# Kernel tuning notes

Hardware: AMD Instinct MI355X
Metric: run time of the kernel (lower is better)

## Reference

```python
import jax, jax.numpy as jnp
import numpy as np

B, N, FEAT, HID, CTX = 16384, 7, 512, 256, 256
COMB = N * HID + CTX  # 2048


def setup_inputs() -> dict:
    key = jax.random.key(0)
    ks = jax.random.split(key, 20)
    s = lambda k, shape, sc=0.05: jax.random.normal(k, shape, dtype=jnp.float32) * sc
    adj = jax.random.randint(ks[1], (N, N), 0, 2).astype(jnp.float32)
    # guarantee self-loops so no row is fully masked (still exercise nan_to_num path robustly)
    adj = jnp.maximum(adj, jnp.eye(N, dtype=jnp.float32))
    return {
        "node_feats": jax.random.normal(ks[0], (B, N, FEAT), dtype=jnp.float32),
        "adj": adj,
        "context": jax.random.normal(ks[2], (B, CTX), dtype=jnp.float32),
        "base_preds": jax.random.normal(ks[3], (B, 5), dtype=jnp.float32),
        "W1": s(ks[4], (HID, FEAT)),
        "a1": s(ks[5], (1, 2 * HID)),
        "W2": s(ks[6], (HID, HID)),
        "a2": s(ks[7], (1, 2 * HID)),
        "wh1_w": s(ks[8], (32, COMB)), "wh1_b": s(ks[9], (32,)),
        "wh2_w": s(ks[10], (16, 32)), "wh2_b": s(ks[11], (16,)),
        "wh3_w": s(ks[12], (5, 16)), "wh3_b": s(ks[13], (5,)),
        "rh1_w": s(ks[14], (16, COMB)), "rh1_b": s(ks[15], (16,)),
        "rh2_w": s(ks[16], (1, 16)), "rh2_b": s(ks[17], (1,)),
    }


def _gat_layer(x, adj, W, a):
    # x: (B, N, in_dim); W: (D, in_dim); a: (1, 2D)
    h = jnp.einsum('bni,di->bnd', x, W)  # (B, N, D)
    D = W.shape[0]
    # a([h_i, h_j]) == h_i @ a[:, :D] + h_j @ a[:, D:]
    s_i = h @ a[0, :D]   # (B, N)
    s_j = h @ a[0, D:]   # (B, N)
    e = s_i[:, :, None] + s_j[:, None, :]          # (B, N, N)
    e = jax.nn.leaky_relu(e, negative_slope=0.2)
    e = jnp.where(adj[None] == 0, -jnp.inf, e)
    alpha = jax.nn.softmax(e, axis=-1)
    alpha = jnp.nan_to_num(alpha, nan=0.0)
    out = jnp.einsum('bij,bjd->bid', alpha, h)     # (B, N, D)
    return out, alpha


def reference(node_feats, adj, context, base_preds, W1, a1, W2, a2,
              wh1_w, wh1_b, wh2_w, wh2_b, wh3_w, wh3_b,
              rh1_w, rh1_b, rh2_w, rh2_b):
    h, _attn1 = _gat_layer(node_feats, adj, W1, a1)
    h = jax.nn.relu(h)
    h, attn2 = _gat_layer(h, adj, W2, a2)
    h = jax.nn.relu(h)
    graph_embed = h.reshape(h.shape[0], -1)                 # (B, N*D)
    combined = jnp.concatenate([graph_embed, context], -1)  # (B, COMB)
    # weight head (dropout is inference-mode identity)
    t = jax.nn.relu(combined @ wh1_w.T + wh1_b)
    t = jax.nn.relu(t @ wh2_w.T + wh2_b)
    raw_weights = t @ wh3_w.T + wh3_b                       # (B, 5)
    weights = jax.nn.softmax(raw_weights, axis=-1)
    weighted_pred = jnp.sum(weights * base_preds, axis=-1)  # (B,)
    r = jnp.tanh(combined @ rh1_w.T + rh1_b)
    residual = (r @ rh2_w.T + rh2_b)[:, 0] * 0.05
    pred = jnp.maximum(weighted_pred + residual, 0.05)
    return pred, weights, attn2
```

## Files before the change

### kernel.cpp

```cpp
#include <hip/hip_runtime.h>

#define B_SZ 16384
#define NN 7
#define HID 256
#define COMB 2048

typedef __attribute__((ext_vector_type(8))) short short8;
typedef __attribute__((ext_vector_type(4))) float floatx4;
typedef __attribute__((ext_vector_type(4))) unsigned short ushortx4;
typedef unsigned short us;

__device__ __forceinline__ float bf2f(us u) {
    union { unsigned int i; float f; } v; v.i = ((unsigned int)u) << 16; return v.f;
}
__device__ __forceinline__ us f2bf(float f) {
    union { unsigned int i; float f; } v; v.f = f;
    return (us)((v.i + 0x7FFFu + ((v.i >> 16) & 1u)) >> 16);
}
__device__ __forceinline__ us f2bf_fast(float f) {
    union { unsigned int i; float f; } v; v.f = f;
    return (us)((v.i + 0x8000u) >> 16);
}
__device__ __forceinline__ void gl_lds16(const us* g, us* l) {
    __builtin_amdgcn_global_load_lds(
        (const __attribute__((address_space(1))) unsigned int*)g,
        (__attribute__((address_space(3))) unsigned int*)l, 16, 0, 0);
}

__global__ __launch_bounds__(256) void pack_weights(const float* __restrict__ W1,
                                                    const float* __restrict__ W2,
                                                    const float* __restrict__ wh1,
                                                    const float* __restrict__ rh1,
                                                    us* __restrict__ dst) {
    int i = (blockIdx.x * 256 + threadIdx.x) * 4;
    if (i >= 294912) return;
    const float* src; int off;
    if (i < 131072)      { src = W1;  off = i; }
    else if (i < 196608) { src = W2;  off = i - 131072; }
    else if (i < 262144) { src = wh1; off = i - 196608; }
    else                 { src = rh1; off = i - 262144; }
    floatx4 v = *(const floatx4*)(src + off);
    ushortx4 o = {f2bf(v[0]), f2bf(v[1]), f2bf(v[2]), f2bf(v[3])};
    *(ushortx4*)(dst + i) = o;
}

template <int SRC_STRIDE, bool WRITE_ALPHA>
__device__ __forceinline__ void attn_graph(const us* hb, const float* adjs, const float* avec,
                                           us* dst, int dstStride, float* alpha_dst, int lane) {
    float hv[NN][4];
#pragma unroll
    for (int n = 0; n < NN; ++n) {
        ushortx4 r = *(const ushortx4*)(hb + n * SRC_STRIDE + lane * 4);
        hv[n][0] = bf2f(r[0]); hv[n][1] = bf2f(r[1]);
        hv[n][2] = bf2f(r[2]); hv[n][3] = bf2f(r[3]);
    }
    floatx4 ai = *(const floatx4*)(avec + lane * 4);
    floatx4 aj = *(const floatx4*)(avec + HID + lane * 4);
    float si[NN], sj[NN];
#pragma unroll
    for (int n = 0; n < NN; ++n) {
        float pi = hv[n][0] * ai[0] + hv[n][1] * ai[1] + hv[n][2] * ai[2] + hv[n][3] * ai[3];
        float pj = hv[n][0] * aj[0] + hv[n][1] * aj[1] + hv[n][2] * aj[2] + hv[n][3] * aj[3];
#pragma unroll
        for (int off = 32; off; off >>= 1) {
            pi += __shfl_xor(pi, off);
            pj += __shfl_xor(pj, off);
        }
        si[n] = pi; sj[n] = pj;
    }
    const int j = lane & 7;
    float sjm = sj[0];
    if (j == 1) sjm = sj[1];
    if (j == 2) sjm = sj[2];
    if (j == 3) sjm = sj[3];
    if (j == 4) sjm = sj[4];
    if (j == 5) sjm = sj[5];
    if (j == 6) sjm = sj[6];
    const int jc = (j < 7) ? j : 0;
    float alpha[NN];
#pragma unroll
    for (int i = 0; i < NN; ++i) {
        float x = si[i] + sjm;
        x = (x >= 0.f) ? x : 0.2f * x;
        bool ok = (j < 7) && (adjs[i * 7 + jc] != 0.f);
        float e = ok ? x : -1e30f;
        float m = e;
        m = fmaxf(m, __shfl_xor(m, 1, 8));
        m = fmaxf(m, __shfl_xor(m, 2, 8));
        m = fmaxf(m, __shfl_xor(m, 4, 8));
        float ex = ok ? __expf(e - m) : 0.f;
        float s = ex;
        s += __shfl_xor(s, 1, 8);
        s += __shfl_xor(s, 2, 8);
        s += __shfl_xor(s, 4, 8);
        alpha[i] = (s > 0.f) ? ex * __frcp_rn(s) : 0.f;
    }
    if (WRITE_ALPHA && lane < 7) {
#pragma unroll
        for (int i = 0; i < NN; ++i) alpha_dst[i * NN + lane] = alpha[i];
    }
#pragma unroll
    for (int i = 0; i < NN; ++i) {
        floatx4 o = (floatx4){0.f, 0.f, 0.f, 0.f};
#pragma unroll
        for (int jj = 0; jj < NN; ++jj) {
            float a = __shfl(alpha[i], jj, 8);
            o[0] += a * hv[jj][0]; o[1] += a * hv[jj][1];
            o[2] += a * hv[jj][2]; o[3] += a * hv[jj][3];
        }
        ushortx4 st = {f2bf(fmaxf(o[0], 0.f)), f2bf(fmaxf(o[1], 0.f)),
                       f2bf(fmaxf(o[2], 0.f)), f2bf(fmaxf(o[3], 0.f))};
        *(ushortx4*)(dst + i * dstStride + lane * 4) = st;
    }
}

__global__ __launch_bounds__(512) void fused_g1(const float* __restrict__ Af,
                                                const us* __restrict__ W1b,
                                                const float* __restrict__ adj,
                                                const float* __restrict__ avec,
                                                us* __restrict__ x2g) {
    extern __shared__ __attribute__((aligned(16))) char smem[];
    us* As = (us*)smem;
    us* Bs = (us*)(smem + 7168);
    us* hs = (us*)(smem + 23552);
    float* adjs = (float*)(smem + 80896);

    const int tid = threadIdx.x;
    const int wave = tid >> 6, lane = tid & 63;
    const int quad = lane >> 4, m16 = lane & 15;
    const long rowBase = (long)blockIdx.x * 112;
    if (tid < 49) adjs[tid] = adj[tid];

    floatx4 acc[7][2];
#pragma unroll
    for (int rt = 0; rt < 7; ++rt)
#pragma unroll
        for (int ct = 0; ct < 2; ++ct) acc[rt][ct] = (floatx4){0.f, 0.f, 0.f, 0.f};

    for (int k0 = 0; k0 < 512; k0 += 32) {
        if (tid < 448) {
            int r = tid >> 2, kh = tid & 3;
            const floatx4* src = (const floatx4*)(Af + (rowBase + r) * 512 + k0 + kh * 8);
            floatx4 v0 = src[0], v1 = src[1];
            short8 s;
            s[0] = f2bf_fast(v0[0]); s[1] = f2bf_fast(v0[1]);
            s[2] = f2bf_fast(v0[2]); s[3] = f2bf_fast(v0[3]);
            s[4] = f2bf_fast(v1[0]); s[5] = f2bf_fast(v1[1]);
            s[6] = f2bf_fast(v1[2]); s[7] = f2bf_fast(v1[3]);
            *(short8*)&As[(r >> 4) * 512 + (kh * 16 + (r & 15)) * 8] = s;
        }
        {
            int b1 = wave * 16, b2 = 128 + wave * 16;
            gl_lds16(W1b + (long)(b1 + (lane & 15)) * 512 + k0 + (lane >> 4) * 8, &Bs[b1 * 32]);
            gl_lds16(W1b + (long)(b2 + (lane & 15)) * 512 + k0 + (lane >> 4) * 8, &Bs[b2 * 32]);
        }
        __syncthreads();
        short8 af[7], bf[2];
#pragma unroll
        for (int rt = 0; rt < 7; ++rt)
            af[rt] = *(const short8*)&As[rt * 512 + (quad * 16 + m16) * 8];
#pragma unroll
        for (int ct = 0; ct < 2; ++ct)
            bf[ct] = *(const short8*)&Bs[(wave * 2 + ct) * 512 + (quad * 16 + m16) * 8];
#pragma unroll
        for (int rt = 0; rt < 7; ++rt)
#pragma unroll
            for (int ct = 0; ct < 2; ++ct)
                acc[rt][ct] = __builtin_amdgcn_mfma_f32_16x16x32_bf16(af[rt], bf[ct], acc[rt][ct], 0, 0, 0);
        __syncthreads();
    }
#pragma unroll
    for (int rt = 0; rt < 7; ++rt)
#pragma unroll
        for (int ct = 0; ct < 2; ++ct)
#pragma unroll
            for (int i = 0; i < 4; ++i)
                hs[(rt * 16 + quad * 4 + i) * 256 + wave * 32 + ct * 16 + m16] = f2bf(acc[rt][ct][i]);
    __syncthreads();
#pragma unroll
    for (int gg = 0; gg < 2; ++gg) {
        int gl = wave * 2 + gg;
        long b = (long)blockIdx.x * 16 + gl;
        attn_graph<256, false>(&hs[gl * 7 * 256], adjs, avec,
                               x2g + b * 7 * 256, 256, nullptr, lane);
    }
}

__global__ __launch_bounds__(512) void fused_rest(const us* __restrict__ x2g,
                                                  const us* __restrict__ W2b,
                                                  const us* __restrict__ Whb,
                                                  const float* __restrict__ adj,
                                                  const float* __restrict__ avec,
                                                  const float* __restrict__ context,
                                                  const float* __restrict__ wh1_b,
                                                  const float* __restrict__ wh2_w,
                                                  const float* __restrict__ wh2_b,
                                                  const float* __restrict__ wh3_w,
                                                  const float* __restrict__ wh3_b,
                                                  const float* __restrict__ rh1_b,
                                                  const float* __restrict__ rh2_w,
                                                  const float* __restrict__ rh2_b,
                                                  const float* __restrict__ base_preds,
                                                  float* __restrict__ out) {
    extern __shared__ __attribute__((aligned(16))) char smem[];
    us* As = (us*)smem;
    us* Bs = (us*)(smem + 8192);
    us* hs = (us*)(smem + 24576);
    us* ctxs = (us*)(smem + 82816);
    float* red = (float*)(smem + 91136);
    float* fin = (float*)(smem + 115712);
    float* adjs = (float*)(smem + 118784);

    const int tid = threadIdx.x;
    const int wave = tid >> 6, lane = tid & 63;
    const int quad = lane >> 4, m16 = lane & 15;
    const long rowBase = (long)blockIdx.x * 112;
    const long gbase = (long)blockIdx.x * 16;
    if (tid < 49) adjs[tid] = adj[tid];
    {
        int r = tid >> 5, c = (tid & 31) * 8;
        const floatx4* src = (const floatx4*)(context + (gbase + r) * 256 + c);
        floatx4 v0 = src[0], v1 = src[1];
        short8 s;
        s[0] = f2bf(v0[0]); s[1] = f2bf(v0[1]); s[2] = f2bf(v0[2]); s[3] = f2bf(v0[3]);
        s[4] = f2bf(v1[0]); s[5] = f2bf(v1[1]); s[6] = f2bf(v1[2]); s[7] = f2bf(v1[3]);
        *(short8*)&ctxs[r * 260 + c] = s;
    }

    floatx4 acc[7][2];
#pragma unroll
    for (int rt = 0; rt < 7; ++rt)
#pragma unroll
        for (int ct = 0; ct < 2; ++ct) acc[rt][ct] = (floatx4){0.f, 0.f, 0.f, 0.f};

    for (int k0 = 0; k0 < 256; k0 += 32) {
        gl_lds16(x2g + (rowBase + wave * 16 + (lane & 15)) * 256 + k0 + (lane >> 4) * 8,
                 &As[wave * 512]);
        {
            int b1 = wave * 16, b2 = 128 + wave * 16;
            gl_lds16(W2b + (long)(b1 + (lane & 15)) * 256 + k0 + (lane >> 4) * 8, &Bs[b1 * 32]);
            gl_lds16(W2b + (long)(b2 + (lane & 15)) * 256 + k0 + (lane >> 4) * 8, &Bs[b2 * 32]);
        }
        __syncthreads();
        short8 af[7], bf[2];
#pragma unroll
        for (int rt = 0; rt < 7; ++rt)
            af[rt] = *(const short8*)&As[rt * 512 + (quad * 16 + m16) * 8];
#pragma unroll
        for (int ct = 0; ct < 2; ++ct)
            bf[ct] = *(const short8*)&Bs[(wave * 2 + ct) * 512 + (quad * 16 + m16) * 8];
#pragma unroll
        for (int rt = 0; rt < 7; ++rt)
#pragma unroll
            for (int ct = 0; ct < 2; ++ct)
                acc[rt][ct] = __builtin_amdgcn_mfma_f32_16x16x32_bf16(af[rt], bf[ct], acc[rt][ct], 0, 0, 0);
        __syncthreads();
    }
#pragma unroll
    for (int rt = 0; rt < 7; ++rt)
#pragma unroll
        for (int ct = 0; ct < 2; ++ct)
#pragma unroll
            for (int i = 0; i < 4; ++i)
                hs[(rt * 16 + quad * 4 + i) * 260 + wave * 32 + ct * 16 + m16] = f2bf(acc[rt][ct][i]);
    __syncthreads();
    float* alf = out + 6 * B_SZ;
#pragma unroll
    for (int gg = 0; gg < 2; ++gg) {
        int gl = wave * 2 + gg;
        long b = gbase + gl;
        attn_graph<260, true>(&hs[gl * 7 * 260], adjs, avec,
                              &hs[gl * 7 * 260], 260, alf + b * 49, lane);
    }
    __syncthreads();
    floatx4 acc3[3];
#pragma unroll
    for (int ct = 0; ct < 3; ++ct) acc3[ct] = (floatx4){0.f, 0.f, 0.f, 0.f};
    const long wk = (long)wave * 256;
#pragma unroll
    for (int s = 0; s < 8; ++s) {
        int kk = s * 32;
        short8 a;
        if (wave < 7) a = *(const short8*)&hs[(m16 * 7 + wave) * 260 + kk + quad * 8];
        else          a = *(const short8*)&ctxs[m16 * 260 + kk + quad * 8];
#pragma unroll
        for (int ct = 0; ct < 3; ++ct) {
            short8 bh = *(const short8*)(Whb + (long)(ct * 16 + m16) * COMB + wk + kk + quad * 8);
            acc3[ct] = __builtin_amdgcn_mfma_f32_16x16x32_bf16(a, bh, acc3[ct], 0, 0, 0);
        }
    }
#pragma unroll
    for (int ct = 0; ct < 3; ++ct)
#pragma unroll
        for (int i = 0; i < 4; ++i)
            red[wave * 768 + (quad * 4 + i) * 48 + ct * 16 + m16] = acc3[ct][i];
    __syncthreads();
    {
        float s = 0.f;
#pragma unroll
        for (int w = 0; w < 8; ++w) s += red[w * 768 + tid];
        fin[tid] = s;
        if (tid < 256) {
            float s2 = 0.f;
#pragma unroll
            for (int w = 0; w < 8; ++w) s2 += red[w * 768 + 512 + tid];
            fin[512 + tid] = s2;
        }
    }
    __syncthreads();
    if (tid < 16) {
        const int g = tid;
        const long b = gbase + g;
        const float* g48 = &fin[g * 48];
        float t1[32], r1[16];
#pragma unroll
        for (int k = 0; k < 32; ++k) t1[k] = fmaxf(g48[k] + wh1_b[k], 0.f);
#pragma unroll
        for (int k = 0; k < 16; ++k) r1[k] = tanhf(g48[32 + k] + rh1_b[k]);
        float t2[16];
#pragma unroll
        for (int jj = 0; jj < 16; ++jj) {
            float s = wh2_b[jj];
            for (int k = 0; k < 32; ++k) s += wh2_w[jj * 32 + k] * t1[k];
            t2[jj] = fmaxf(s, 0.f);
        }
        float rw[5], m = -1e30f;
#pragma unroll
        for (int o = 0; o < 5; ++o) {
            float s = wh3_b[o];
            for (int jj = 0; jj < 16; ++jj) s += wh3_w[o * 16 + jj] * t2[jj];
            rw[o] = s; m = fmaxf(m, s);
        }
        float se = 0.f;
#pragma unroll
        for (int o = 0; o < 5; ++o) { rw[o] = __expf(rw[o] - m); se += rw[o]; }
        float inv = 1.f / se, wp = 0.f;
#pragma unroll
        for (int o = 0; o < 5; ++o) {
            float w = rw[o] * inv;
            out[B_SZ + b * 5 + o] = w;
            wp += w * base_preds[b * 5 + o];
        }
        float rs = rh2_b[0];
#pragma unroll
        for (int k = 0; k < 16; ++k) rs += rh2_w[k] * r1[k];
        out[b] = fmaxf(wp + rs * 0.05f, 0.05f);
    }
}

extern "C" void kernel_launch(void* const* d_in, const int* in_sizes, int n_in,
                              void* d_out, int out_size, void* d_ws, size_t ws_size,
                              hipStream_t stream) {
    const float* node_feats = (const float*)d_in[0];
    const float* adj        = (const float*)d_in[1];
    const float* context    = (const float*)d_in[2];
    const float* base_preds = (const float*)d_in[3];
    const float* W1         = (const float*)d_in[4];
    const float* a1         = (const float*)d_in[5];
    const float* W2         = (const float*)d_in[6];
    const float* a2         = (const float*)d_in[7];
    const float* wh1_w = (const float*)d_in[8];
    const float* wh1_b = (const float*)d_in[9];
    const float* wh2_w = (const float*)d_in[10];
    const float* wh2_b = (const float*)d_in[11];
    const float* wh3_w = (const float*)d_in[12];
    const float* wh3_b = (const float*)d_in[13];
    const float* rh1_w = (const float*)d_in[14];
    const float* rh1_b = (const float*)d_in[15];
    const float* rh2_w = (const float*)d_in[16];
    const float* rh2_b = (const float*)d_in[17];
    float* out = (float*)d_out;

    char* ws = (char*)d_ws;
    const size_t HB = (size_t)B_SZ * NN * HID * 2;
    us* x2  = (us*)ws;
    us* W1b = (us*)(ws + HB);
    us* W2b = W1b + 131072;
    us* Whb = W2b + 65536;

    pack_weights<<<288, 256, 0, stream>>>(W1, W2, wh1_w, rh1_w, W1b);

    fused_g1<<<1024, 512, 81104, stream>>>(node_feats, W1b, adj, a1, x2);

    fused_rest<<<1024, 512, 118992, stream>>>(x2, W2b, Whb, adj, a2, context,
                                              wh1_b, wh2_w, wh2_b, wh3_w, wh3_b,
                                              rh1_b, rh2_w, rh2_b, base_preds, out);
}
```

Before: 541.7 us.

## Halve per-block tile to 8 graphs, read weights from global, raise occupancy

Both fused kernels now process 8 graphs (56 rows) per block instead of 16, over twice as many blocks. LDS use drops sharply: weight tiles are no longer staged in shared memory and each wave reads its B fragments straight from global/L2. The K step grows to 64 and launch bounds request 4 blocks per CU. The aim is more resident waves to hide memory latency, at the cost of more redundant global weight reads and a 64-row MFMA tile where only 56 rows are useful.

```diff
diff --git a/kernel.cpp b/kernel.cpp
--- a/kernel.cpp
+++ b/kernel.cpp
@@ -114,204 +114,185 @@
     }
 }
 
-__global__ __launch_bounds__(512) void fused_g1(const float* __restrict__ Af,
-                                                const us* __restrict__ W1b,
-                                                const float* __restrict__ adj,
-                                                const float* __restrict__ avec,
-                                                us* __restrict__ x2g) {
-    extern __shared__ __attribute__((aligned(16))) char smem[];
-    us* As = (us*)smem;
-    us* Bs = (us*)(smem + 7168);
-    us* hs = (us*)(smem + 23552);
-    float* adjs = (float*)(smem + 80896);
-
+
+__global__ __launch_bounds__(512, 4) void fused_g1(const float* __restrict__ Af,
+                                                   const us* __restrict__ W1b,
+                                                   const float* __restrict__ adj,
+                                                   const float* __restrict__ avec,
+                                                   us* __restrict__ x2g) {
+    __shared__ __attribute__((aligned(16))) us As[4096];
+    __shared__ __attribute__((aligned(16))) us hs[56 * 264];
+    __shared__ float adjs[52];
     const int tid = threadIdx.x;
     const int wave = tid >> 6, lane = tid & 63;
     const int quad = lane >> 4, m16 = lane & 15;
-    const long rowBase = (long)blockIdx.x * 112;
+    const long rowBase = (long)blockIdx.x * 56;
     if (tid < 49) adjs[tid] = adj[tid];
 
-    floatx4 acc[7][2];
-#pragma unroll
-    for (int rt = 0; rt < 7; ++rt)
+    floatx4 acc[4][2];
+#pragma unroll
+    for (int rt = 0; rt < 4; ++rt)
 #pragma unroll
         for (int ct = 0; ct < 2; ++ct) acc[rt][ct] = (floatx4){0.f, 0.f, 0.f, 0.f};
 
-    for (int k0 = 0; k0 < 512; k0 += 32) {
-        if (tid < 448) {
-            int r = tid >> 2, kh = tid & 3;
-            const floatx4* src = (const floatx4*)(Af + (rowBase + r) * 512 + k0 + kh * 8);
-            floatx4 v0 = src[0], v1 = src[1];
-            short8 s;
-            s[0] = f2bf_fast(v0[0]); s[1] = f2bf_fast(v0[1]);
-            s[2] = f2bf_fast(v0[2]); s[3] = f2bf_fast(v0[3]);
-            s[4] = f2bf_fast(v1[0]); s[5] = f2bf_fast(v1[1]);
-            s[6] = f2bf_fast(v1[2]); s[7] = f2bf_fast(v1[3]);
-            *(short8*)&As[(r >> 4) * 512 + (kh * 16 + (r & 15)) * 8] = s;
-        }
-        {
-            int b1 = wave * 16, b2 = 128 + wave * 16;
-            gl_lds16(W1b + (long)(b1 + (lane & 15)) * 512 + k0 + (lane >> 4) * 8, &Bs[b1 * 32]);
-            gl_lds16(W1b + (long)(b2 + (lane & 15)) * 512 + k0 + (lane >> 4) * 8, &Bs[b2 * 32]);
-        }
+    const int r = tid >> 3, kq8 = tid & 7;
+    long rowA = rowBase + r; if (rowA > 114687) rowA = 114687;
+    const float* aptr = Af + rowA * 512 + kq8 * 8;
+    us* wdst = &As[((r >> 3) * 64 + (r & 7) * 8 + kq8) * 8];
+    const int colb = wave * 32;
+
+    for (int s = 0; s < 8; ++s) {
+        const int k0 = s * 64;
+        floatx4 v0 = *(const floatx4*)(aptr + k0);
+        floatx4 v1 = *(const floatx4*)(aptr + k0 + 4);
+        short8 sv;
+        sv[0] = f2bf_fast(v0[0]); sv[1] = f2bf_fast(v0[1]);
+        sv[2] = f2bf_fast(v0[2]); sv[3] = f2bf_fast(v0[3]);
+        sv[4] = f2bf_fast(v1[0]); sv[5] = f2bf_fast(v1[1]);
+        sv[6] = f2bf_fast(v1[2]); sv[7] = f2bf_fast(v1[3]);
+        *(short8*)wdst = sv;
         __syncthreads();
-        short8 af[7], bf[2];
-#pragma unroll
-        for (int rt = 0; rt < 7; ++rt)
-            af[rt] = *(const short8*)&As[rt * 512 + (quad * 16 + m16) * 8];
+#pragma unroll
+        for (int t = 0; t < 2; ++t) {
+            short8 b0 = *(const short8*)(W1b + (long)(colb + m16) * 512 + k0 + t * 32 + quad * 8);
+            short8 b1 = *(const short8*)(W1b + (long)(colb + 16 + m16) * 512 + k0 + t * 32 + quad * 8);
+            short8 a[4];
+#pragma unroll
+            for (int rt = 0; rt < 4; ++rt)
+                a[rt] = *(const short8*)&As[((rt * 2 + (m16 >> 3)) * 64 + (m16 & 7) * 8 + t * 4 + quad) * 8];
+#pragma unroll
+            for (int rt = 0; rt < 4; ++rt) {
+                acc[rt][0] = __builtin_amdgcn_mfma_f32_16x16x32_bf16(a[rt], b0, acc[rt][0], 0, 0, 0);
+                acc[rt][1] = __builtin_amdgcn_mfma_f32_16x16x32_bf16(a[rt], b1, acc[rt][1], 0, 0, 0);
+            }
+        }
+        __syncthreads();
+    }
+#pragma unroll
+    for (int rt = 0; rt < 4; ++rt)
 #pragma unroll
         for (int ct = 0; ct < 2; ++ct)
-            bf[ct] = *(const short8*)&Bs[(wave * 2 + ct) * 512 + (quad * 16 + m16) * 8];
-#pragma unroll
-        for (int rt = 0; rt < 7; ++rt)
-#pragma unroll
-            for (int ct = 0; ct < 2; ++ct)
-                acc[rt][ct] = __builtin_amdgcn_mfma_f32_16x16x32_bf16(af[rt], bf[ct], acc[rt][ct], 0, 0, 0);
-        __syncthreads();
-    }
-#pragma unroll
-    for (int rt = 0; rt < 7; ++rt)
-#pragma unroll
-        for (int ct = 0; ct < 2; ++ct)
-#pragma unroll
-            for (int i = 0; i < 4; ++i)
-                hs[(rt * 16 + quad * 4 + i) * 256 + wave * 32 + ct * 16 + m16] = f2bf(acc[rt][ct][i]);
-    __syncthreads();
-#pragma unroll
-    for (int gg = 0; gg < 2; ++gg) {
-        int gl = wave * 2 + gg;
-        long b = (long)blockIdx.x * 16 + gl;
-        attn_graph<256, false>(&hs[gl * 7 * 256], adjs, avec,
-                               x2g + b * 7 * 256, 256, nullptr, lane);
-    }
-}
-
-__global__ __launch_bounds__(512) void fused_rest(const us* __restrict__ x2g,
-                                                  const us* __restrict__ W2b,
-                                                  const us* __restrict__ Whb,
-                                                  const float* __restrict__ adj,
-                                                  const float* __restrict__ avec,
-                                                  const float* __restrict__ context,
-                                                  const float* __restrict__ wh1_b,
-                                                  const float* __restrict__ wh2_w,
-                                                  const float* __restrict__ wh2_b,
-                                                  const float* __restrict__ wh3_w,
-                                                  const float* __restrict__ wh3_b,
-                                                  const float* __restrict__ rh1_b,
-                                                  const float* __restrict__ rh2_w,
-                                                  const float* __restrict__ rh2_b,
-                                                  const float* __restrict__ base_preds,
-                                                  float* __restrict__ out) {
-    extern __shared__ __attribute__((aligned(16))) char smem[];
-    us* As = (us*)smem;
-    us* Bs = (us*)(smem + 8192);
-    us* hs = (us*)(smem + 24576);
-    us* ctxs = (us*)(smem + 82816);
-    float* red = (float*)(smem + 91136);
-    float* fin = (float*)(smem + 115712);
-    float* adjs = (float*)(smem + 118784);
-
+#pragma unroll
+            for (int i = 0; i < 4; ++i) {
+                int row = rt * 16 + quad * 4 + i;
+                if (row < 56) hs[row * 264 + wave * 32 + ct * 16 + m16] = f2bf(acc[rt][ct][i]);
+            }
+    __syncthreads();
+    attn_graph<264, false>(&hs[wave * 7 * 264], adjs, avec,
+                           x2g + ((long)blockIdx.x * 64 + wave * 7) * 256, 256, nullptr, lane);
+}
+
+__global__ __launch_bounds__(512, 4) void fused_rest(const us* __restrict__ x2g,
+                                                     const us* __restrict__ W2b,
+                                                     const us* __restrict__ Whb,
+                                                     const float* __restrict__ adj,
+                                                     const float* __restrict__ avec,
+                                                     const float* __restrict__ context,
+                                                     const float* __restrict__ wh1_b,
+                                                     const float* __restrict__ wh2_w,
+                                                     const float* __restrict__ wh2_b,
+                                                     const float* __restrict__ wh3_w,
+                                                     const float* __restrict__ wh3_b,
+                                                     const float* __restrict__ rh1_b,
+                                                     const float* __restrict__ rh2_w,
+                                                     const float* __restrict__ rh2_b,
+                                                     const float* __restrict__ base_preds,
+                                                     float* __restrict__ out) {
+    __shared__ __attribute__((aligned(16))) us As[4096];
+    __shared__ __attribute__((aligned(16))) us hs[56 * 264];
+    __shared__ __attribute__((aligned(16))) us ctxs[8 * 264];
+    __shared__ float red[8 * 384];
+    __shared__ float fin[384];
+    __shared__ float adjs[52];
     const int tid = threadIdx.x;
     const int wave = tid >> 6, lane = tid & 63;
     const int quad = lane >> 4, m16 = lane & 15;
-    const long rowBase = (long)blockIdx.x * 112;
-    const long gbase = (long)blockIdx.x * 16;
+    const long rowBaseX = (long)blockIdx.x * 64;
+    const long gbase = (long)blockIdx.x * 8;
     if (tid < 49) adjs[tid] = adj[tid];
     {
-        int r = tid >> 5, c = (tid & 31) * 8;
-        const floatx4* src = (const floatx4*)(context + (gbase + r) * 256 + c);
-        floatx4 v0 = src[0], v1 = src[1];
-        short8 s;
-        s[0] = f2bf(v0[0]); s[1] = f2bf(v0[1]); s[2] = f2bf(v0[2]); s[3] = f2bf(v0[3]);
-        s[4] = f2bf(v1[0]); s[5] = f2bf(v1[1]); s[6] = f2bf(v1[2]); s[7] = f2bf(v1[3]);
-        *(short8*)&ctxs[r * 260 + c] = s;
-    }
-
-    floatx4 acc[7][2];
-#pragma unroll
-    for (int rt = 0; rt < 7; ++rt)
+        int cr = tid >> 6, c4 = (tid & 63) * 4;
+        floatx4 cv = *(const floatx4*)(context + (gbase + cr) * 256 + c4);
+        ushortx4 st = {f2bf(cv[0]), f2bf(cv[1]), f2bf(cv[2]), f2bf(cv[3])};
+        *(ushortx4*)&ctxs[cr * 264 + c4] = st;
+    }
+
+    floatx4 acc[4][2];
+#pragma unroll
+    for (int rt = 0; rt < 4; ++rt)
 #pragma unroll
         for (int ct = 0; ct < 2; ++ct) acc[rt][ct] = (floatx4){0.f, 0.f, 0.f, 0.f};
-
-    for (int k0 = 0; k0 < 256; k0 += 32) {
-        gl_lds16(x2g + (rowBase + wave * 16 + (lane & 15)) * 256 + k0 + (lane >> 4) * 8,
+    const int colb = wave * 32;
+
+    for (int s = 0; s < 4; ++s) {
+        const int k0 = s * 64;
+        gl_lds16(x2g + (rowBaseX + wave * 8 + (lane >> 3)) * 256 + k0 + (lane & 7) * 8,
                  &As[wave * 512]);
-        {
-            int b1 = wave * 16, b2 = 128 + wave * 16;
-            gl_lds16(W2b + (long)(b1 + (lane & 15)) * 256 + k0 + (lane >> 4) * 8, &Bs[b1 * 32]);
-            gl_lds16(W2b + (long)(b2 + (lane & 15)) * 256 + k0 + (lane >> 4) * 8, &Bs[b2 * 32]);
-        }
         __syncthreads();
-        short8 af[7], bf[2];
-#pragma unroll
-        for (int rt = 0; rt < 7; ++rt)
-            af[rt] = *(const short8*)&As[rt * 512 + (quad * 16 + m16) * 8];
+#pragma unroll
+        for (int t = 0; t < 2; ++t) {
+            short8 b0 = *(const short8*)(W2b + (long)(colb + m16) * 256 + k0 + t * 32 + quad * 8);
+            short8 b1 = *(const short8*)(W2b + (long)(colb + 16 + m16) * 256 + k0 + t * 32 + quad * 8);
+            short8 a[4];
+#pragma unroll
+            for (int rt = 0; rt < 4; ++rt)
+                a[rt] = *(const short8*)&As[((rt * 2 + (m16 >> 3)) * 64 + (m16 & 7) * 8 + t * 4 + quad) * 8];
+#pragma unroll
+            for (int rt = 0; rt < 4; ++rt) {
+                acc[rt][0] = __builtin_amdgcn_mfma_f32_16x16x32_bf16(a[rt], b0, acc[rt][0], 0, 0, 0);
+                acc[rt][1] = __builtin_amdgcn_mfma_f32_16x16x32_bf16(a[rt], b1, acc[rt][1], 0, 0, 0);
+            }
+        }
+        __syncthreads();
+    }
+#pragma unroll
+    for (int rt = 0; rt < 4; ++rt)
 #pragma unroll
         for (int ct = 0; ct < 2; ++ct)
-            bf[ct] = *(const short8*)&Bs[(wave * 2 + ct) * 512 + (quad * 16 + m16) * 8];
-#pragma unroll
-        for (int rt = 0; rt < 7; ++rt)
-#pragma unroll
-            for (int ct = 0; ct < 2; ++ct)
-                acc[rt][ct] = __builtin_amdgcn_mfma_f32_16x16x32_bf16(af[rt], bf[ct], acc[rt][ct], 0, 0, 0);
-        __syncthreads();
-    }
-#pragma unroll
-    for (int rt = 0; rt < 7; ++rt)
-#pragma unroll
-        for (int ct = 0; ct < 2; ++ct)
-#pragma unroll
-            for (int i = 0; i < 4; ++i)
-                hs[(rt * 16 + quad * 4 + i) * 260 + wave * 32 + ct * 16 + m16] = f2bf(acc[rt][ct][i]);
+#pragma unroll
+            for (int i = 0; i < 4; ++i) {
+                int row = rt * 16 + quad * 4 + i;
+                if (row < 56) hs[row * 264 + wave * 32 + ct * 16 + m16] = f2bf(acc[rt][ct][i]);
+            }
     __syncthreads();
     float* alf = out + 6 * B_SZ;
-#pragma unroll
-    for (int gg = 0; gg < 2; ++gg) {
-        int gl = wave * 2 + gg;
-        long b = gbase + gl;
-        attn_graph<260, true>(&hs[gl * 7 * 260], adjs, avec,
-                              &hs[gl * 7 * 260], 260, alf + b * 49, lane);
-    }
+    attn_graph<264, true>(&hs[wave * 7 * 264], adjs, avec,
+                          &hs[wave * 7 * 264], 264, alf + (gbase + wave) * 49, lane);
     __syncthreads();
     floatx4 acc3[3];
 #pragma unroll
     for (int ct = 0; ct < 3; ++ct) acc3[ct] = (floatx4){0.f, 0.f, 0.f, 0.f};
-    const long wk = (long)wave * 256;
-#pragma unroll
-    for (int s = 0; s < 8; ++s) {
-        int kk = s * 32;
+    const int g = m16 & 7;
+#pragma unroll
+    for (int s2 = 0; s2 < 8; ++s2) {
+        const int kk = s2 * 32;
         short8 a;
-        if (wave < 7) a = *(const short8*)&hs[(m16 * 7 + wave) * 260 + kk + quad * 8];
-        else          a = *(const short8*)&ctxs[m16 * 260 + kk + quad * 8];
+        if (wave < 7) a = *(const short8*)&hs[(g * 7 + wave) * 264 + kk + quad * 8];
+        else          a = *(const short8*)&ctxs[g * 264 + kk + quad * 8];
 #pragma unroll
         for (int ct = 0; ct < 3; ++ct) {
-            short8 bh = *(const short8*)(Whb + (long)(ct * 16 + m16) * COMB + wk + kk + quad * 8);
+            short8 bh = *(const short8*)(Whb + (long)(ct * 16 + m16) * COMB + wave * 256 + kk + quad * 8);
             acc3[ct] = __builtin_amdgcn_mfma_f32_16x16x32_bf16(a, bh, acc3[ct], 0, 0, 0);
         }
     }
 #pragma unroll
     for (int ct = 0; ct < 3; ++ct)
 #pragma unroll
-        for (int i = 0; i < 4; ++i)
-            red[wave * 768 + (quad * 4 + i) * 48 + ct * 16 + m16] = acc3[ct][i];
-    __syncthreads();
-    {
-        float s = 0.f;
-#pragma unroll
-        for (int w = 0; w < 8; ++w) s += red[w * 768 + tid];
-        fin[tid] = s;
-        if (tid < 256) {
-            float s2 = 0.f;
-#pragma unroll
-            for (int w = 0; w < 8; ++w) s2 += red[w * 768 + 512 + tid];
-            fin[512 + tid] = s2;
-        }
-    }
-    __syncthreads();
-    if (tid < 16) {
-        const int g = tid;
-        const long b = gbase + g;
-        const float* g48 = &fin[g * 48];
+        for (int i = 0; i < 4; ++i) {
+            int g2 = quad * 4 + i;
+            if (g2 < 8) red[wave * 384 + g2 * 48 + ct * 16 + m16] = acc3[ct][i];
+        }
+    __syncthreads();
+    if (tid < 384) {
+        float ssum = 0.f;
+#pragma unroll
+        for (int w = 0; w < 8; ++w) ssum += red[w * 384 + tid];
+        fin[tid] = ssum;
+    }
+    __syncthreads();
+    if (tid < 8) {
+        const long b = gbase + tid;
+        const float* g48 = &fin[tid * 48];
         float t1[32], r1[16];
 #pragma unroll
         for (int k = 0; k < 32; ++k) t1[k] = fmaxf(g48[k] + wh1_b[k], 0.f);
@@ -372,17 +353,17 @@
     float* out = (float*)d_out;
 
     char* ws = (char*)d_ws;
-    const size_t HB = (size_t)B_SZ * NN * HID * 2;
+    const size_t X2B = (size_t)2048 * 64 * 256 * 2;
     us* x2  = (us*)ws;
-    us* W1b = (us*)(ws + HB);
+    us* W1b = (us*)(ws + X2B);
     us* W2b = W1b + 131072;
     us* Whb = W2b + 65536;
 
     pack_weights<<<288, 256, 0, stream>>>(W1, W2, wh1_w, rh1_w, W1b);
 
-    fused_g1<<<1024, 512, 81104, stream>>>(node_feats, W1b, adj, a1, x2);
-
-    fused_rest<<<1024, 512, 118992, stream>>>(x2, W2b, Whb, adj, a2, context,
-                                              wh1_b, wh2_w, wh2_b, wh3_w, wh3_b,
-                                              rh1_b, rh2_w, rh2_b, base_preds, out);
-}
+    fused_g1<<<2048, 512, 0, stream>>>(node_feats, W1b, adj, a1, x2);
+
+    fused_rest<<<2048, 512, 0, stream>>>(x2, W2b, Whb, adj, a2, context,
+                                         wh1_b, wh2_w, wh2_b, wh3_w, wh3_b,
+                                         rh1_b, rh2_w, rh2_b, base_preds, out);
+}
```

Measured after the change: 540.8 us. No clear change (-0.2%).
